# Kernel tuning notes

Hardware: AMD Instinct MI355X
Metric: run time of the kernel (lower is better)

Reference implementation:

```python
import jax, jax.numpy as jnp
import numpy as np

N = 50000      # nodes in current tree level
N_CH = 3       # actual children present in mailbox
D = 4          # max_output_degree
H = 256        # h_size


def setup_inputs() -> dict:
    key = jax.random.key(0)
    ks = jax.random.split(key, 6)
    return {
        "neighbour_h": jax.random.normal(ks[0], (N, N_CH, H), dtype=jnp.float32),
        "neighbour_c": jax.random.normal(ks[1], (N, N_CH, H), dtype=jnp.float32),
        "f_input": jax.random.normal(ks[2], (N, H), dtype=jnp.float32),
        "iou_input": jax.random.normal(ks[3], (N, 3 * H), dtype=jnp.float32),
        # torch nn.Linear convention: weight [out, in]; one per child position
        "U_f": jax.random.normal(ks[4], (D, H, H), dtype=jnp.float32) * 0.05,
        "U_iou": jax.random.normal(ks[5], (D, 3 * H, H), dtype=jnp.float32) * 0.05,
    }


def reference(neighbour_h, neighbour_c, f_input, iou_input, U_f, U_iou):
    n, n_ch, h = neighbour_h.shape
    d = U_f.shape[0]
    pad = d - n_ch
    # check_missing_children: pad with bottom_h / bottom_c == zeros
    nh = jnp.pad(neighbour_h, ((0, 0), (0, pad), (0, 0)))  # [N, D, H]
    nc = jnp.pad(neighbour_c, ((0, 0), (0, pad), (0, 0)))  # [N, D, H]
    # per-position forget gates: U_f_i @ h_i, plus f_input repeated per child
    f_logits = jnp.einsum('ndh,dkh->ndk', nh, U_f) + f_input[:, None, :]
    # iou gate (canonical n-ary tree-LSTM): sum_i U_iou_i @ h_i, plus iou_input
    iou_aggr = jnp.einsum('ndh,dkh->nk', nh, U_iou) + iou_input  # [N, 3H]
    f = jax.nn.sigmoid(f_logits)
    c_aggr = jnp.sum(f * nc, axis=1)  # [N, H]
    # apply_node_func: iou = iou_input + iou_aggr (iou_input counted twice, as in source)
    iou = iou_input + iou_aggr
    i, o, u = jnp.split(iou, 3, axis=1)
    c = jax.nn.sigmoid(i) * jnp.tanh(u) + c_aggr
    h_out = jax.nn.sigmoid(o) * jnp.tanh(c)
    return (h_out, c)
```

## Files before the change

kernel.cpp:

```cpp
#include <hip/hip_runtime.h>
#include <cstdint>
#include <cstddef>

#define NNODES 50000
#define HD 256
#define NCH 3
#define BM 32

typedef __attribute__((ext_vector_type(8))) short shortx8;
typedef __attribute__((ext_vector_type(4))) float floatx4;
typedef __attribute__((ext_vector_type(16))) float floatx16;

__device__ __forceinline__ unsigned short f2bf(float x) {
    union { float f; uint32_t u; } v; v.f = x;
    uint32_t r = v.u + 0x7fffu + ((v.u >> 16) & 1u);
    return (unsigned short)(r >> 16);
}
__device__ __forceinline__ float bf2f(unsigned short u) {
    union { uint32_t u; float f; } v; v.u = ((uint32_t)u) << 16; return v.f;
}
__device__ __forceinline__ shortx8 cvt8(float4 a, float4 b) {
    shortx8 o;
    o[0] = (short)f2bf(a.x); o[1] = (short)f2bf(a.y);
    o[2] = (short)f2bf(a.z); o[3] = (short)f2bf(a.w);
    o[4] = (short)f2bf(b.x); o[5] = (short)f2bf(b.y);
    o[6] = (short)f2bf(b.z); o[7] = (short)f2bf(b.w);
    return o;
}
__device__ __forceinline__ float sigf(float x) {
    return 1.0f / (1.0f + __expf(-x));
}
__device__ __forceinline__ float tanhfast(float x) {
    return 1.0f - 2.0f / (__expf(2.0f * x) + 1.0f);
}
__device__ __forceinline__ floatx16 mfma32(shortx8 a, shortx8 b, floatx16 c) {
    return __builtin_amdgcn_mfma_f32_32x32x16_bf16(a, b, c, 0, 0, 0);
}

__global__ void prep_weights32(const float* __restrict__ U_f,
                               const float* __restrict__ U_iou,
                               unsigned short* __restrict__ wsB) {
    int idx = blockIdx.x * 256 + threadIdx.x;
    int lane = idx & 63;
    int ks   = (idx >> 6) & 15;
    int tile = (idx >> 10) & 31;
    int d    = idx >> 15;
    if (d >= NCH) return;
    int col = tile * 32 + (lane & 31);
    int k0  = ks * 16 + (lane >> 5) * 8;
    const float* src = (col < 256)
        ? (U_f   + (((size_t)d * 256 + col)         * 256 + k0))
        : (U_iou + (((size_t)d * 768 + (col - 256)) * 256 + k0));
    shortx8 o;
    #pragma unroll
    for (int e = 0; e < 8; ++e) o[e] = (short)f2bf(src[e]);
    reinterpret_cast<shortx8*>(wsB)[idx] = o;
}

__global__ __launch_bounds__(512, 4) void treelstm_main(
    const float* __restrict__ nh,
    const float* __restrict__ ncc,
    const float* __restrict__ f_in,
    const float* __restrict__ iou_in,
    const unsigned short* __restrict__ wsB,
    float* __restrict__ out)
{
    __shared__ unsigned short sA[NCH * BM * 32 * 8];

    const int tid  = threadIdx.x;
    const int nb   = blockIdx.x * BM;
    const int lane = tid & 63;
    const int cg   = tid >> 6;
    const int nl   = lane & 31;
    const int hi   = lane >> 5;
    const int colb = cg * 32 + hi * 4;

    const shortx8* Bfr = reinterpret_cast<const shortx8*>(wsB);

    #pragma unroll
    for (int i = 0; i < 6; ++i) {
        int c    = i * 512 + tid;
        int d    = c >> 10;
        int node = (c >> 5) & 31;
        int slot = c & 31;
        int gn   = nb + node;
        shortx8 o;
        if (gn < NNODES) {
            const float4* q = reinterpret_cast<const float4*>(
                nh + ((size_t)gn * (NCH * HD) + d * HD + slot * 8));
            o = cvt8(q[0], q[1]);
        } else {
            #pragma unroll
            for (int e = 0; e < 8; ++e) o[e] = 0;
        }
        int idx = (d * BM + node) * 32 + (slot ^ (node & 7));
        *reinterpret_cast<shortx8*>(&sA[idx * 8]) = o;
    }
    __syncthreads();

    const int  n     = nb + nl;
    const bool valid = (n < NNODES);
    const int  nc_   = valid ? n : (NNODES - 1);

    ushort4 finb[4];
    #pragma unroll
    for (int q = 0; q < 4; ++q) {
        floatx4 v = *reinterpret_cast<const floatx4*>(
            f_in + (size_t)nc_ * HD + colb + q * 8);
        finb[q] = ushort4{f2bf(v[0]), f2bf(v[1]), f2bf(v[2]), f2bf(v[3])};
    }

    float cagg[16];
    #pragma unroll
    for (int t = 0; t < 16; ++t) cagg[t] = 0.0f;

    floatx16 accI, accO, accU;
    #pragma unroll
    for (int t = 0; t < 16; ++t) { accI[t] = 0.0f; accO[t] = 0.0f; accU[t] = 0.0f; }

    const int nsw = nl & 7;

    #pragma unroll 1
    for (int d = 0; d < NCH; ++d) {
        floatx16 accF;
        #pragma unroll
        for (int t = 0; t < 16; ++t) accF[t] = 0.0f;

        #pragma unroll 2
        for (int ks = 0; ks < 16; ++ks) {
            shortx8 aF = Bfr[((d * 32 +      cg) * 16 + ks) * 64 + lane];
            shortx8 aI = Bfr[((d * 32 +  8 + cg) * 16 + ks) * 64 + lane];
            shortx8 aO = Bfr[((d * 32 + 16 + cg) * 16 + ks) * 64 + lane];
            shortx8 aU = Bfr[((d * 32 + 24 + cg) * 16 + ks) * 64 + lane];
            int ch = (ks * 2 + hi) ^ nsw;
            shortx8 b = *reinterpret_cast<const shortx8*>(
                &sA[((d * BM + nl) * 32 + ch) * 8]);
            accF = mfma32(aF, b, accF);
            accI = mfma32(aI, b, accI);
            accO = mfma32(aO, b, accO);
            accU = mfma32(aU, b, accU);
        }

        #pragma unroll
        for (int q = 0; q < 4; ++q) {
            floatx4 ncr = *reinterpret_cast<const floatx4*>(
                ncc + (size_t)nc_ * (NCH * HD) + d * HD + colb + q * 8);
            cagg[q * 4 + 0] += sigf(accF[q * 4 + 0] + bf2f(finb[q].x)) * ncr[0];
            cagg[q * 4 + 1] += sigf(accF[q * 4 + 1] + bf2f(finb[q].y)) * ncr[1];
            cagg[q * 4 + 2] += sigf(accF[q * 4 + 2] + bf2f(finb[q].z)) * ncr[2];
            cagg[q * 4 + 3] += sigf(accF[q * 4 + 3] + bf2f(finb[q].w)) * ncr[3];
        }
    }

    if (valid) {
        #pragma unroll
        for (int q = 0; q < 4; ++q) {
            int col = colb + q * 8;
            size_t base = (size_t)n * 768 + col;
            floatx4 i4 = *reinterpret_cast<const floatx4*>(iou_in + base);
            floatx4 o4 = *reinterpret_cast<const floatx4*>(iou_in + base + 256);
            floatx4 u4 = *reinterpret_cast<const floatx4*>(iou_in + base + 512);
            floatx4 cc, hh;
            #pragma unroll
            for (int r = 0; r < 4; ++r) {
                int t = q * 4 + r;
                float iv = accI[t] + 2.0f * i4[r];
                float ov = accO[t] + 2.0f * o4[r];
                float uv = accU[t] + 2.0f * u4[r];
                float c  = sigf(iv) * tanhfast(uv) + cagg[t];
                cc[r] = c;
                hh[r] = sigf(ov) * tanhfast(c);
            }
            *reinterpret_cast<floatx4*>(out + (size_t)n * HD + col) = hh;
            *reinterpret_cast<floatx4*>(out + (size_t)(NNODES + n) * HD + col) = cc;
        }
    }
}

extern "C" void kernel_launch(void* const* d_in, const int* in_sizes, int n_in,
                              void* d_out, int out_size, void* d_ws, size_t ws_size,
                              hipStream_t stream) {
    const float* nh     = (const float*)d_in[0];
    const float* ncc    = (const float*)d_in[1];
    const float* f_in   = (const float*)d_in[2];
    const float* iou_in = (const float*)d_in[3];
    const float* U_f    = (const float*)d_in[4];
    const float* U_iou  = (const float*)d_in[5];
    unsigned short* wsB = (unsigned short*)d_ws;

    if (ws_size < (size_t)(3 * 32 * 16 * 64) * 16) return;

    hipLaunchKernelGGL(prep_weights32, dim3(384), dim3(256), 0, stream,
                       U_f, U_iou, wsB);
    hipLaunchKernelGGL(treelstm_main, dim3((NNODES + BM - 1) / BM), dim3(512),
                       0, stream, nh, ncc, f_in, iou_in, wsB, (float*)d_out);
}
```

Measured before the change: 283.5 us.

## Double node tile to 64 with 1024-thread blocks and packed bf16 conversion

Each block now covers 64 nodes with 16 waves, two node groups sharing the same weight column tiles, so weight fragment traffic per node is meant to be amortised over a larger tile. The fp32-to-bf16 conversion of the neighbour hidden states now uses the packed v_cvt_pk_bf16_f32 instruction instead of manual rounding. f_input is now read in fp32 inside the per-child loop rather than kept as bf16 registers, which changes precision slightly. The larger block uses dynamic shared memory and drops the occupancy hint, which may reduce the number of resident blocks per CU.

```diff
diff --git a/kernel.cpp b/kernel.cpp
--- a/kernel.cpp
+++ b/kernel.cpp
@@ -5,7 +5,7 @@
 #define NNODES 50000
 #define HD 256
 #define NCH 3
-#define BM 32
+#define BM 64
 
 typedef __attribute__((ext_vector_type(8))) short shortx8;
 typedef __attribute__((ext_vector_type(4))) float floatx4;
@@ -16,16 +16,18 @@
     uint32_t r = v.u + 0x7fffu + ((v.u >> 16) & 1u);
     return (unsigned short)(r >> 16);
 }
-__device__ __forceinline__ float bf2f(unsigned short u) {
-    union { uint32_t u; float f; } v; v.u = ((uint32_t)u) << 16; return v.f;
+__device__ __forceinline__ uint32_t cvtpk(float a, float b) {
+    uint32_t r;
+    asm("v_cvt_pk_bf16_f32 %0, %1, %2" : "=v"(r) : "v"(a), "v"(b));
+    return r;
 }
 __device__ __forceinline__ shortx8 cvt8(float4 a, float4 b) {
-    shortx8 o;
-    o[0] = (short)f2bf(a.x); o[1] = (short)f2bf(a.y);
-    o[2] = (short)f2bf(a.z); o[3] = (short)f2bf(a.w);
-    o[4] = (short)f2bf(b.x); o[5] = (short)f2bf(b.y);
-    o[6] = (short)f2bf(b.z); o[7] = (short)f2bf(b.w);
-    return o;
+    union { uint32_t u[4]; shortx8 v; } o;
+    o.u[0] = cvtpk(a.x, a.y);
+    o.u[1] = cvtpk(a.z, a.w);
+    o.u[2] = cvtpk(b.x, b.y);
+    o.u[3] = cvtpk(b.z, b.w);
+    return o.v;
 }
 __device__ __forceinline__ float sigf(float x) {
     return 1.0f / (1.0f + __expf(-x));
@@ -57,7 +59,7 @@
     reinterpret_cast<shortx8*>(wsB)[idx] = o;
 }
 
-__global__ __launch_bounds__(512, 4) void treelstm_main(
+__global__ __launch_bounds__(1024) void treelstm_main(
     const float* __restrict__ nh,
     const float* __restrict__ ncc,
     const float* __restrict__ f_in,
@@ -65,25 +67,28 @@
     const unsigned short* __restrict__ wsB,
     float* __restrict__ out)
 {
-    __shared__ unsigned short sA[NCH * BM * 32 * 8];
+    extern __shared__ unsigned short sA[];
 
     const int tid  = threadIdx.x;
     const int nb   = blockIdx.x * BM;
     const int lane = tid & 63;
-    const int cg   = tid >> 6;
+    const int w    = tid >> 6;
+    const int cg   = w & 7;
+    const int nt   = w >> 3;
     const int nl   = lane & 31;
     const int hi   = lane >> 5;
     const int colb = cg * 32 + hi * 4;
+    const int node = nt * 32 + nl;
 
     const shortx8* Bfr = reinterpret_cast<const shortx8*>(wsB);
 
     #pragma unroll
     for (int i = 0; i < 6; ++i) {
-        int c    = i * 512 + tid;
-        int d    = c >> 10;
-        int node = (c >> 5) & 31;
-        int slot = c & 31;
-        int gn   = nb + node;
+        int c     = i * 1024 + tid;
+        int d     = c >> 11;
+        int nodeS = (c >> 5) & 63;
+        int slot  = c & 31;
+        int gn    = nb + nodeS;
         shortx8 o;
         if (gn < NNODES) {
             const float4* q = reinterpret_cast<const float4*>(
@@ -93,22 +98,14 @@
             #pragma unroll
             for (int e = 0; e < 8; ++e) o[e] = 0;
         }
-        int idx = (d * BM + node) * 32 + (slot ^ (node & 7));
+        int idx = (d * BM + nodeS) * 32 + (slot ^ (nodeS & 7));
         *reinterpret_cast<shortx8*>(&sA[idx * 8]) = o;
     }
     __syncthreads();
 
-    const int  n     = nb + nl;
+    const int  n     = nb + node;
     const bool valid = (n < NNODES);
     const int  nc_   = valid ? n : (NNODES - 1);
-
-    ushort4 finb[4];
-    #pragma unroll
-    for (int q = 0; q < 4; ++q) {
-        floatx4 v = *reinterpret_cast<const floatx4*>(
-            f_in + (size_t)nc_ * HD + colb + q * 8);
-        finb[q] = ushort4{f2bf(v[0]), f2bf(v[1]), f2bf(v[2]), f2bf(v[3])};
-    }
 
     float cagg[16];
     #pragma unroll
@@ -118,7 +115,7 @@
     #pragma unroll
     for (int t = 0; t < 16; ++t) { accI[t] = 0.0f; accO[t] = 0.0f; accU[t] = 0.0f; }
 
-    const int nsw = nl & 7;
+    const int nsw = node & 7;
 
     #pragma unroll 1
     for (int d = 0; d < NCH; ++d) {
@@ -134,7 +131,7 @@
             shortx8 aU = Bfr[((d * 32 + 24 + cg) * 16 + ks) * 64 + lane];
             int ch = (ks * 2 + hi) ^ nsw;
             shortx8 b = *reinterpret_cast<const shortx8*>(
-                &sA[((d * BM + nl) * 32 + ch) * 8]);
+                &sA[((d * BM + node) * 32 + ch) * 8]);
             accF = mfma32(aF, b, accF);
             accI = mfma32(aI, b, accI);
             accO = mfma32(aO, b, accO);
@@ -145,10 +142,12 @@
         for (int q = 0; q < 4; ++q) {
             floatx4 ncr = *reinterpret_cast<const floatx4*>(
                 ncc + (size_t)nc_ * (NCH * HD) + d * HD + colb + q * 8);
-            cagg[q * 4 + 0] += sigf(accF[q * 4 + 0] + bf2f(finb[q].x)) * ncr[0];
-            cagg[q * 4 + 1] += sigf(accF[q * 4 + 1] + bf2f(finb[q].y)) * ncr[1];
-            cagg[q * 4 + 2] += sigf(accF[q * 4 + 2] + bf2f(finb[q].z)) * ncr[2];
-            cagg[q * 4 + 3] += sigf(accF[q * 4 + 3] + bf2f(finb[q].w)) * ncr[3];
+            floatx4 fi4 = *reinterpret_cast<const floatx4*>(
+                f_in + (size_t)nc_ * HD + colb + q * 8);
+            #pragma unroll
+            for (int r = 0; r < 4; ++r)
+                cagg[q * 4 + r] +=
+                    sigf(accF[q * 4 + r] + fi4[r]) * ncr[r];
         }
     }
 
@@ -192,6 +191,7 @@
 
     hipLaunchKernelGGL(prep_weights32, dim3(384), dim3(256), 0, stream,
                        U_f, U_iou, wsB);
-    hipLaunchKernelGGL(treelstm_main, dim3((NNODES + BM - 1) / BM), dim3(512),
-                       0, stream, nh, ncc, f_in, iou_in, wsB, (float*)d_out);
+    hipLaunchKernelGGL(treelstm_main, dim3((NNODES + BM - 1) / BM), dim3(1024),
+                       NCH * BM * 32 * 8 * sizeof(unsigned short), stream,
+                       nh, ncc, f_in, iou_in, wsB, (float*)d_out);
 }
```

New measurement: 313.3 us. +10.5%, slower.

## Split into tiled GEMM writing bf16 logits plus separate elementwise kernel

Applied to the files above, without the earlier changes.

Replaces the single fused kernel with a two-stage pipeline. A 128-node tiled GEMM, double-buffered through LDS, writes bf16 forget and iou logits to workspace in chunks, and an elementwise kernel then applies the gates and combines the results. The iou weights are laid out as one K=768 GEMM so each tile reuses weight fragments across four node subtiles, and bf16 conversion uses the packed v_cvt_pk_bf16_f32 instruction. The cost is an extra global round trip of the logits, which are also rounded to bf16, and the fused path is kept as a fallback when the workspace is too small.

```diff
diff --git a/kernel.cpp b/kernel.cpp
--- a/kernel.cpp
+++ b/kernel.cpp
@@ -2,10 +2,9 @@
 #include <cstdint>
 #include <cstddef>
 
-#define NNODES 50000
+#define NN 50000
 #define HD 256
 #define NCH 3
-#define BM 32
 
 typedef __attribute__((ext_vector_type(8))) short shortx8;
 typedef __attribute__((ext_vector_type(4))) float floatx4;
@@ -19,13 +18,10 @@
 __device__ __forceinline__ float bf2f(unsigned short u) {
     union { uint32_t u; float f; } v; v.u = ((uint32_t)u) << 16; return v.f;
 }
-__device__ __forceinline__ shortx8 cvt8(float4 a, float4 b) {
-    shortx8 o;
-    o[0] = (short)f2bf(a.x); o[1] = (short)f2bf(a.y);
-    o[2] = (short)f2bf(a.z); o[3] = (short)f2bf(a.w);
-    o[4] = (short)f2bf(b.x); o[5] = (short)f2bf(b.y);
-    o[6] = (short)f2bf(b.z); o[7] = (short)f2bf(b.w);
-    return o;
+__device__ __forceinline__ uint32_t cvtpk(float a, float b) {
+    uint32_t r;
+    asm("v_cvt_pk_bf16_f32 %0, %1, %2" : "=v"(r) : "v"(a), "v"(b));
+    return r;
 }
 __device__ __forceinline__ float sigf(float x) {
     return 1.0f / (1.0f + __expf(-x));
@@ -37,9 +33,188 @@
     return __builtin_amdgcn_mfma_f32_32x32x16_bf16(a, b, c, 0, 0, 0);
 }
 
-__global__ void prep_weights32(const float* __restrict__ U_f,
-                               const float* __restrict__ U_iou,
-                               unsigned short* __restrict__ wsB) {
+__global__ void prep_split(const float* __restrict__ U_f,
+                           const float* __restrict__ U_iou,
+                           unsigned short* __restrict__ wsB) {
+    int idx  = blockIdx.x * 256 + threadIdx.x;
+    int lane = idx & 63;
+    int fg   = idx >> 6;
+    const float* src;
+    if (fg < 384) {
+        int t   = fg >> 4;
+        int ksl = fg & 15;
+        int d   = t >> 3;
+        int c   = t * 32 + (lane & 31) - d * 256;
+        int kk  = ksl * 16 + (lane >> 5) * 8;
+        src = U_f + ((size_t)d * 256 + c) * 256 + kk;
+    } else {
+        int fg2 = fg - 384;
+        int t2  = fg2 / 48;
+        int ksl = fg2 % 48;
+        int gc  = t2 * 32 + (lane & 31);
+        int g   = gc >> 8;
+        int c   = gc & 255;
+        int k   = ksl * 16 + (lane >> 5) * 8;
+        int d   = k >> 8;
+        int kk  = k & 255;
+        src = U_iou + ((size_t)d * 768 + g * 256 + c) * 256 + kk;
+    }
+    shortx8 o;
+    #pragma unroll
+    for (int e = 0; e < 8; ++e) o[e] = (short)f2bf(src[e]);
+    reinterpret_cast<shortx8*>(wsB)[idx] = o;
+}
+
+__global__ __launch_bounds__(256, 4) void gemm_logits(
+    const float* __restrict__ nh,
+    const unsigned short* __restrict__ wsB,
+    unsigned short* __restrict__ logits,
+    int node_base, int count)
+{
+    __shared__ unsigned short sA[2][128 * 64];
+
+    const int tid = threadIdx.x;
+    const int bid = blockIdx.x;
+    const int cb  = bid % 12;
+    const int mb  = bid / 12;
+    const int nb  = node_base + mb * 128;
+
+    const int lane = tid & 63;
+    const int cg   = tid >> 6;
+    const int nl   = lane & 31;
+    const int hi   = lane >> 5;
+    const int swz  = nl & 7;
+
+    const bool isF   = (cb < 6);
+    const int  dch   = cb >> 1;
+    const int  kbase = isF ? dch * 256 : 0;
+    const int  nsteps = isF ? 4 : 12;
+    const int  tF  = cb * 4 + cg;
+    const int  t2  = (cb - 6) * 4 + cg;
+    const int  fragbase = isF ? (tF * 16) : (384 + t2 * 48);
+    const int  colbase  = (isF ? (tF * 32) : (768 + t2 * 32)) + hi * 4;
+
+    const shortx8* Bfr = reinterpret_cast<const shortx8*>(wsB);
+
+    floatx16 acc[4];
+    #pragma unroll
+    for (int nt = 0; nt < 4; ++nt)
+        #pragma unroll
+        for (int t = 0; t < 16; ++t) acc[nt][t] = 0.0f;
+
+#define STAGE(S, B)                                                          \
+    {                                                                        \
+        _Pragma("unroll 4")                                                  \
+        for (int i = 0; i < 8; ++i) {                                        \
+            int flat = i * 256 + tid;                                        \
+            int node = flat >> 4;                                            \
+            int kc   = flat & 15;                                            \
+            int gn   = nb + node;                                            \
+            uint2 wv; wv.x = 0u; wv.y = 0u;                                  \
+            if (gn < NN) {                                                   \
+                float4 v = *reinterpret_cast<const float4*>(                 \
+                    nh + (size_t)gn * (NCH * HD) + kbase + (S) * 64 + kc * 4);\
+                wv.x = cvtpk(v.x, v.y);                                      \
+                wv.y = cvtpk(v.z, v.w);                                      \
+            }                                                                \
+            int byt = node * 128 + (((kc >> 1) ^ (node & 7)) * 16)           \
+                      + (kc & 1) * 8;                                        \
+            *reinterpret_cast<uint2*>(                                       \
+                reinterpret_cast<char*>(&sA[(B)][0]) + byt) = wv;            \
+        }                                                                    \
+    }
+
+    STAGE(0, 0);
+    __syncthreads();
+    for (int s = 0; s < nsteps; ++s) {
+        if (s + 1 < nsteps) STAGE(s + 1, (s + 1) & 1);
+        const unsigned short* buf = &sA[s & 1][0];
+        #pragma unroll
+        for (int it = 0; it < 4; ++it) {
+            shortx8 a = Bfr[(fragbase + s * 4 + it) * 64 + lane];
+            int ch = (it * 2 + hi) ^ swz;
+            #pragma unroll
+            for (int nt = 0; nt < 4; ++nt) {
+                shortx8 b = *reinterpret_cast<const shortx8*>(
+                    buf + (nt * 32 + nl) * 64 + ch * 8);
+                acc[nt] = mfma32(a, b, acc[nt]);
+            }
+        }
+        __syncthreads();
+    }
+#undef STAGE
+
+    #pragma unroll
+    for (int nt = 0; nt < 4; ++nt) {
+        int gn = nb + nt * 32 + nl;
+        if (gn < node_base + count) {
+            unsigned short* lr = logits + (size_t)(gn - node_base) * 1536;
+            #pragma unroll
+            for (int q = 0; q < 4; ++q) {
+                uint2 wv;
+                wv.x = cvtpk(acc[nt][q * 4 + 0], acc[nt][q * 4 + 1]);
+                wv.y = cvtpk(acc[nt][q * 4 + 2], acc[nt][q * 4 + 3]);
+                *reinterpret_cast<uint2*>(lr + colbase + q * 8) = wv;
+            }
+        }
+    }
+}
+
+__global__ __launch_bounds__(256) void ew_kernel(
+    const unsigned short* __restrict__ logits,
+    const float* __restrict__ ncc,
+    const float* __restrict__ f_in,
+    const float* __restrict__ iou_in,
+    float* __restrict__ out,
+    int node_base, int count)
+{
+    int total = count * 64;
+    for (int id = blockIdx.x * 256 + threadIdx.x; id < total;
+         id += gridDim.x * 256) {
+        int row = id >> 6;
+        int col = (id & 63) * 4;
+        int gn  = node_base + row;
+        const unsigned short* lr = logits + (size_t)row * 1536;
+
+        floatx4 fi = *reinterpret_cast<const floatx4*>(
+            f_in + (size_t)gn * HD + col);
+        float cagg[4] = {0.f, 0.f, 0.f, 0.f};
+        #pragma unroll
+        for (int d = 0; d < 3; ++d) {
+            ushort4 fb = *reinterpret_cast<const ushort4*>(lr + d * 256 + col);
+            floatx4 nc4 = *reinterpret_cast<const floatx4*>(
+                ncc + (size_t)gn * 768 + d * 256 + col);
+            cagg[0] += sigf(bf2f(fb.x) + fi[0]) * nc4[0];
+            cagg[1] += sigf(bf2f(fb.y) + fi[1]) * nc4[1];
+            cagg[2] += sigf(bf2f(fb.z) + fi[2]) * nc4[2];
+            cagg[3] += sigf(bf2f(fb.w) + fi[3]) * nc4[3];
+        }
+        ushort4 ib = *reinterpret_cast<const ushort4*>(lr +  768 + col);
+        ushort4 ob = *reinterpret_cast<const ushort4*>(lr + 1024 + col);
+        ushort4 ub = *reinterpret_cast<const ushort4*>(lr + 1280 + col);
+        size_t iob = (size_t)gn * 768 + col;
+        floatx4 i4 = *reinterpret_cast<const floatx4*>(iou_in + iob);
+        floatx4 o4 = *reinterpret_cast<const floatx4*>(iou_in + iob + 256);
+        floatx4 u4 = *reinterpret_cast<const floatx4*>(iou_in + iob + 512);
+        float iv[4] = {bf2f(ib.x), bf2f(ib.y), bf2f(ib.z), bf2f(ib.w)};
+        float ov[4] = {bf2f(ob.x), bf2f(ob.y), bf2f(ob.z), bf2f(ob.w)};
+        float uv[4] = {bf2f(ub.x), bf2f(ub.y), bf2f(ub.z), bf2f(ub.w)};
+        floatx4 cc, hh;
+        #pragma unroll
+        for (int r = 0; r < 4; ++r) {
+            float c = sigf(iv[r] + 2.0f * i4[r]) * tanhfast(uv[r] + 2.0f * u4[r])
+                      + cagg[r];
+            cc[r] = c;
+            hh[r] = sigf(ov[r] + 2.0f * o4[r]) * tanhfast(c);
+        }
+        *reinterpret_cast<floatx4*>(out + (size_t)gn * HD + col) = hh;
+        *reinterpret_cast<floatx4*>(out + (size_t)(NN + gn) * HD + col) = cc;
+    }
+}
+
+__global__ void prep_fused32(const float* __restrict__ U_f,
+                             const float* __restrict__ U_iou,
+                             unsigned short* __restrict__ wsB) {
     int idx = blockIdx.x * 256 + threadIdx.x;
     int lane = idx & 63;
     int ks   = (idx >> 6) & 15;
@@ -57,51 +232,44 @@
     reinterpret_cast<shortx8*>(wsB)[idx] = o;
 }
 
-__global__ __launch_bounds__(512, 4) void treelstm_main(
-    const float* __restrict__ nh,
-    const float* __restrict__ ncc,
-    const float* __restrict__ f_in,
-    const float* __restrict__ iou_in,
-    const unsigned short* __restrict__ wsB,
-    float* __restrict__ out)
+__global__ __launch_bounds__(512, 4) void fused_main(
+    const float* __restrict__ nh, const float* __restrict__ ncc,
+    const float* __restrict__ f_in, const float* __restrict__ iou_in,
+    const unsigned short* __restrict__ wsB, float* __restrict__ out)
 {
-    __shared__ unsigned short sA[NCH * BM * 32 * 8];
-
+    __shared__ unsigned short sA[NCH * 32 * 32 * 8];
     const int tid  = threadIdx.x;
-    const int nb   = blockIdx.x * BM;
+    const int nb   = blockIdx.x * 32;
     const int lane = tid & 63;
     const int cg   = tid >> 6;
     const int nl   = lane & 31;
     const int hi   = lane >> 5;
     const int colb = cg * 32 + hi * 4;
-
     const shortx8* Bfr = reinterpret_cast<const shortx8*>(wsB);
-
     #pragma unroll
     for (int i = 0; i < 6; ++i) {
-        int c    = i * 512 + tid;
-        int d    = c >> 10;
-        int node = (c >> 5) & 31;
-        int slot = c & 31;
-        int gn   = nb + node;
+        int c = i * 512 + tid;
+        int d = c >> 10, node = (c >> 5) & 31, slot = c & 31;
+        int gn = nb + node;
         shortx8 o;
-        if (gn < NNODES) {
+        if (gn < NN) {
             const float4* q = reinterpret_cast<const float4*>(
                 nh + ((size_t)gn * (NCH * HD) + d * HD + slot * 8));
-            o = cvt8(q[0], q[1]);
+            float4 a = q[0], b = q[1];
+            union { uint32_t u[4]; shortx8 v; } t;
+            t.u[0] = cvtpk(a.x, a.y); t.u[1] = cvtpk(a.z, a.w);
+            t.u[2] = cvtpk(b.x, b.y); t.u[3] = cvtpk(b.z, b.w);
+            o = t.v;
         } else {
-            #pragma unroll
             for (int e = 0; e < 8; ++e) o[e] = 0;
         }
-        int idx = (d * BM + node) * 32 + (slot ^ (node & 7));
+        int idx = (d * 32 + node) * 32 + (slot ^ (node & 7));
         *reinterpret_cast<shortx8*>(&sA[idx * 8]) = o;
     }
     __syncthreads();
-
     const int  n     = nb + nl;
-    const bool valid = (n < NNODES);
-    const int  nc_   = valid ? n : (NNODES - 1);
-
+    const bool valid = (n < NN);
+    const int  nc_   = valid ? n : (NN - 1);
     ushort4 finb[4];
     #pragma unroll
     for (int q = 0; q < 4; ++q) {
@@ -109,23 +277,18 @@
             f_in + (size_t)nc_ * HD + colb + q * 8);
         finb[q] = ushort4{f2bf(v[0]), f2bf(v[1]), f2bf(v[2]), f2bf(v[3])};
     }
-
     float cagg[16];
     #pragma unroll
     for (int t = 0; t < 16; ++t) cagg[t] = 0.0f;
-
     floatx16 accI, accO, accU;
     #pragma unroll
-    for (int t = 0; t < 16; ++t) { accI[t] = 0.0f; accO[t] = 0.0f; accU[t] = 0.0f; }
-
+    for (int t = 0; t < 16; ++t) { accI[t] = 0.f; accO[t] = 0.f; accU[t] = 0.f; }
     const int nsw = nl & 7;
-
     #pragma unroll 1
     for (int d = 0; d < NCH; ++d) {
         floatx16 accF;
         #pragma unroll
         for (int t = 0; t < 16; ++t) accF[t] = 0.0f;
-
         #pragma unroll 2
         for (int ks = 0; ks < 16; ++ks) {
             shortx8 aF = Bfr[((d * 32 +      cg) * 16 + ks) * 64 + lane];
@@ -134,24 +297,22 @@
             shortx8 aU = Bfr[((d * 32 + 24 + cg) * 16 + ks) * 64 + lane];
             int ch = (ks * 2 + hi) ^ nsw;
             shortx8 b = *reinterpret_cast<const shortx8*>(
-                &sA[((d * BM + nl) * 32 + ch) * 8]);
+                &sA[((d * 32 + nl) * 32 + ch) * 8]);
             accF = mfma32(aF, b, accF);
             accI = mfma32(aI, b, accI);
             accO = mfma32(aO, b, accO);
             accU = mfma32(aU, b, accU);
         }
-
         #pragma unroll
         for (int q = 0; q < 4; ++q) {
             floatx4 ncr = *reinterpret_cast<const floatx4*>(
                 ncc + (size_t)nc_ * (NCH * HD) + d * HD + colb + q * 8);
-            cagg[q * 4 + 0] += sigf(accF[q * 4 + 0] + bf2f(finb[q].x)) * ncr[0];
-            cagg[q * 4 + 1] += sigf(accF[q * 4 + 1] + bf2f(finb[q].y)) * ncr[1];
-            cagg[q * 4 + 2] += sigf(accF[q * 4 + 2] + bf2f(finb[q].z)) * ncr[2];
-            cagg[q * 4 + 3] += sigf(accF[q * 4 + 3] + bf2f(finb[q].w)) * ncr[3];
-        }
-    }
-
+            cagg[q*4+0] += sigf(accF[q*4+0] + bf2f(finb[q].x)) * ncr[0];
+            cagg[q*4+1] += sigf(accF[q*4+1] + bf2f(finb[q].y)) * ncr[1];
+            cagg[q*4+2] += sigf(accF[q*4+2] + bf2f(finb[q].z)) * ncr[2];
+            cagg[q*4+3] += sigf(accF[q*4+3] + bf2f(finb[q].w)) * ncr[3];
+        }
+    }
     if (valid) {
         #pragma unroll
         for (int q = 0; q < 4; ++q) {
@@ -164,15 +325,13 @@
             #pragma unroll
             for (int r = 0; r < 4; ++r) {
                 int t = q * 4 + r;
-                float iv = accI[t] + 2.0f * i4[r];
-                float ov = accO[t] + 2.0f * o4[r];
-                float uv = accU[t] + 2.0f * u4[r];
-                float c  = sigf(iv) * tanhfast(uv) + cagg[t];
+                float c = sigf(accI[t] + 2.f*i4[r]) * tanhfast(accU[t] + 2.f*u4[r])
+                          + cagg[t];
                 cc[r] = c;
-                hh[r] = sigf(ov) * tanhfast(c);
+                hh[r] = sigf(accO[t] + 2.f*o4[r]) * tanhfast(c);
             }
             *reinterpret_cast<floatx4*>(out + (size_t)n * HD + col) = hh;
-            *reinterpret_cast<floatx4*>(out + (size_t)(NNODES + n) * HD + col) = cc;
+            *reinterpret_cast<floatx4*>(out + (size_t)(NN + n) * HD + col) = cc;
         }
     }
 }
@@ -188,10 +347,37 @@
     const float* U_iou  = (const float*)d_in[5];
     unsigned short* wsB = (unsigned short*)d_ws;
 
-    if (ws_size < (size_t)(3 * 32 * 16 * 64) * 16) return;
-
-    hipLaunchKernelGGL(prep_weights32, dim3(384), dim3(256), 0, stream,
-                       U_f, U_iou, wsB);
-    hipLaunchKernelGGL(treelstm_main, dim3((NNODES + BM - 1) / BM), dim3(512),
-                       0, stream, nh, ncc, f_in, iou_in, wsB, (float*)d_out);
-}
+    const size_t FRAG_BYTES  = (size_t)98304 * 16;
+    const size_t LOGITS_OFF  = (size_t)2 << 20;
+
+    long long cmax = 0;
+    if (ws_size > LOGITS_OFF)
+        cmax = (long long)((ws_size - LOGITS_OFF) / 3072);
+    cmax = (cmax / 128) * 128;
+
+    if (cmax >= 128) {
+        hipLaunchKernelGGL(prep_split, dim3(384), dim3(256), 0, stream,
+                           U_f, U_iou, wsB);
+        unsigned short* logits =
+            (unsigned short*)((char*)d_ws + LOGITS_OFF);
+        int base = 0;
+        while (base < NN) {
+            long long rem = NN - base;
+            int count = (int)(rem < cmax ? rem : cmax);
+            int nmb = (count + 127) / 128;
+            hipLaunchKernelGGL(gemm_logits, dim3(nmb * 12), dim3(256), 0,
+                               stream, nh, wsB, logits, base, count);
+            int ewgrid = (count * 64 + 255) / 256;
+            if (ewgrid > 2048) ewgrid = 2048;
+            hipLaunchKernelGGL(ew_kernel, dim3(ewgrid), dim3(256), 0, stream,
+                               logits, ncc, f_in, iou_in, (float*)d_out,
+                               base, count);
+            base += count;
+        }
+    } else if (ws_size >= FRAG_BYTES) {
+        hipLaunchKernelGGL(prep_fused32, dim3(384), dim3(256), 0, stream,
+                           U_f, U_iou, wsB);
+        hipLaunchKernelGGL(fused_main, dim3((NN + 31) / 32), dim3(512), 0,
+                           stream, nh, ncc, f_in, iou_in, wsB, (float*)d_out);
+    }
+}
```

After: 422.5 us. +49.0%, slower.
